# Performance work log

Measured on AMD Instinct MI355X. Metric: run time of the kernel, lower is better.

## Reference

```python
import jax, jax.numpy as jnp
import numpy as np

N = 50000        # nodes
R = 51           # enriched relations (25 fwd + 25 inverse + self-loop)
F_IN = 32        # feat_size
E = 32           # embed_size
C = 16           # num_classes
B = 30           # num_bases
NNZ = 2_000_000  # nonzeros in vertical adjacency


def _xavier(key, shape):
    # mimics nn.init.xavier_uniform_ with gain for relu (sqrt(2))
    fan_in, fan_out = shape[-2], shape[-1]
    a = np.sqrt(2.0) * np.sqrt(6.0 / (fan_in + fan_out))
    return jax.random.uniform(key, shape, jnp.float32, -a, a)


def setup_inputs() -> dict:
    key = jax.random.key(0)
    ks = jax.random.split(key, 8)
    # COO of vertical adjacency, shape (R*N, N)
    rows = jax.random.randint(ks[0], (NNZ,), 0, R * N)
    cols = jax.random.randint(ks[1], (NNZ,), 0, N)
    # row-normalized values: vals = 1 / row_degree  (sum_sparse with rows=True)
    deg = jax.ops.segment_sum(jnp.ones((NNZ,), jnp.float32), rows, num_segments=R * N)
    vals = (1.0 / jnp.maximum(deg, 1.0))[rows]
    features = jax.random.normal(ks[2], (N, F_IN), jnp.float32)
    comps1 = _xavier(ks[3], (R, B))
    bases1 = _xavier(ks[4], (B, F_IN, E))
    comps2 = _xavier(ks[5], (R, B))
    bases2 = _xavier(ks[6], (B, E, C))
    bias1 = jnp.zeros((E,), jnp.float32)
    bias2 = jnp.zeros((C,), jnp.float32)
    return {
        "features": features, "vals": vals,
        "comps1": comps1, "bases1": bases1, "bias1": bias1,
        "comps2": comps2, "bases2": bases2, "bias2": bias2,
        "rows": rows, "cols": cols,
    }


def _spmm(rows, cols, vals, x):
    # (R*N, N) sparse @ (N, f) dense -> (R*N, f)
    return jax.ops.segment_sum(vals[:, None] * x[cols], rows, num_segments=R * N)


def reference(features, vals, comps1, bases1, bias1, comps2, bases2, bias2, rows, cols):
    # layer 1: SpMM then basis-decomposed per-relation mixing
    h = _spmm(rows, cols, vals, features).reshape(R, N, F_IN)   # (r, n, f)
    w1 = jnp.einsum('rb,bfe->rfe', comps1, bases1)              # (r, f, e)
    h = jnp.einsum('rnf,rfe->ne', h, w1)                        # (n, e)
    h = jax.nn.relu(h + bias1)
    # layer 2
    h = _spmm(rows, cols, vals, h).reshape(R, N, E)             # (r, n, e)
    w2 = jnp.einsum('rb,bho->rho', comps2, bases2)              # (r, e, c)
    h = jnp.einsum('rho,rnh->no', w2, h)                        # (n, c)
    return h + bias2
```

## Files before the change

### kernel.cpp

```cpp
#include <hip/hip_runtime.h>

#define NNODES 50000
#define RREL 51
#define FIN 32
#define EDIM 32
#define CDIM 16
#define BB 30
#define NNZ_ 2000000
#define EPB 4096
#define NBUK 391
#define PCAP_MAX 2750128

typedef unsigned int uint32;
typedef unsigned short ushort;
typedef uint32 u32x2 __attribute__((ext_vector_type(2)));
typedef uint32 u32x4 __attribute__((ext_vector_type(4)));
typedef short bf16x8 __attribute__((ext_vector_type(8)));
typedef float f32x4 __attribute__((ext_vector_type(4)));
typedef float f32x16 __attribute__((ext_vector_type(16)));

static __device__ __forceinline__ uint32 pack_bf16x2(float a, float b) {
    uint32 ua = __builtin_bit_cast(uint32, a);
    uint32 ub = __builtin_bit_cast(uint32, b);
    ua += 0x7fffu + ((ua >> 16) & 1u);
    ub += 0x7fffu + ((ub >> 16) & 1u);
    return (ua >> 16) | (ub & 0xffff0000u);
}
static __device__ __forceinline__ ushort bf16_1(float x) {
    uint32 u = __builtin_bit_cast(uint32, x);
    u += 0x7fffu + ((u >> 16) & 1u);
    return (ushort)(u >> 16);
}

__global__ void k_weights2(const float* __restrict__ bases1, const float* __restrict__ bases2,
                           ushort* __restrict__ Wb1, ushort* __restrict__ Wb2) {
    int i = blockIdx.x * 256 + threadIdx.x;
    if (i < 960 * 32) {
        int e = i & 31, k = i >> 5;
        int b = k >> 5, f = k & 31;
        float v = bases1[b * 1024 + f * 32 + e];
        Wb1[((k >> 3) * 32 + e) * 8 + (k & 7)] = bf16_1(v);
    }
    if (i < 960 * 16) {
        int e = i & 15, k = i >> 4;
        int b = k >> 5, h = k & 31;
        float v = bases2[b * 512 + h * 16 + e];
        Wb2[((k >> 3) * 16 + e) * 8 + (k & 7)] = bf16_1(v);
    }
}

__global__ void k_tobf16(const float2* __restrict__ src, uint32* __restrict__ dst, int n2) {
    int i = blockIdx.x * 256 + threadIdx.x;
    if (i < n2) {
        float2 f = src[i];
        dst[i] = pack_bf16x2(f.x, f.y);
    }
}

__global__ __launch_bounds__(1024) void k_bukhist(const int* __restrict__ rows,
                                                  int* __restrict__ buk_cnt) {
    __shared__ int lc[NBUK];
    int t = threadIdx.x;
    if (t < NBUK) lc[t] = 0;
    __syncthreads();
    size_t k = (size_t)blockIdx.x * EPB + (size_t)t * 4;
    int rr[4];
    if (k + 4 <= NNZ_) {
        int4 rw = *(const int4*)(rows + k);
        rr[0] = rw.x; rr[1] = rw.y; rr[2] = rw.z; rr[3] = rw.w;
    } else {
#pragma unroll
        for (int j = 0; j < 4; j++) rr[j] = (k + j < NNZ_) ? rows[k + j] : -1;
    }
#pragma unroll
    for (int j = 0; j < 4; j++)
        if (rr[j] >= 0) {
            int rel = rr[j] / NNODES;
            int dst = rr[j] - rel * NNODES;
            atomicAdd(&lc[dst >> 7], 1);
        }
    __syncthreads();
    if (t < NBUK) atomicAdd(&buk_cnt[t], lc[t]);
}

__global__ void k_scan1(const int* __restrict__ buk_cnt, int* __restrict__ buk_base,
                        int* __restrict__ buk_cur) {
    if (threadIdx.x == 0) {
        int a = 0;
        for (int b = 0; b < NBUK; b++) { buk_base[b] = a; buk_cur[b] = a; a += buk_cnt[b]; }
        buk_base[NBUK] = a;
    }
}

__global__ __launch_bounds__(1024) void k_bucket2(const int* __restrict__ rows,
                                                  const int* __restrict__ cols,
                                                  const float* __restrict__ vals,
                                                  int* __restrict__ buk_cur,
                                                  u32x2* __restrict__ tok8,
                                                  float* __restrict__ sval_b) {
    __shared__ int bukc[NBUK], lb[NBUK], gb[NBUK];
    __shared__ int ssum[1024];
    __shared__ u32x2 st8[EPB];
    __shared__ float sv[EPB];
    int t = threadIdx.x;
    size_t base = (size_t)blockIdx.x * EPB;
    int total = (int)(((size_t)NNZ_ - base < (size_t)EPB) ? ((size_t)NNZ_ - base) : (size_t)EPB);
    if (t < NBUK) bukc[t] = 0;
    __syncthreads();
    size_t k = base + (size_t)t * 4;
    int bv[4]; uint32 tx[4], ty[4]; float vv[4];
    if (k + 4 <= NNZ_) {
        int4 rw = *(const int4*)(rows + k);
        int4 cw = *(const int4*)(cols + k);
        float4 vw = *(const float4*)(vals + k);
        int rr[4] = {rw.x, rw.y, rw.z, rw.w};
        int cc[4] = {cw.x, cw.y, cw.z, cw.w};
        vv[0] = vw.x; vv[1] = vw.y; vv[2] = vw.z; vv[3] = vw.w;
#pragma unroll
        for (int j = 0; j < 4; j++) {
            int rel = rr[j] / NNODES;
            int dst = rr[j] - rel * NNODES;
            bv[j] = dst >> 7;
            tx[j] = (uint32)dst | ((uint32)rel << 16);
            ty[j] = (uint32)cc[j] | ((uint32)rel << 16);
        }
    } else {
#pragma unroll
        for (int j = 0; j < 4; j++) {
            if (k + j < NNZ_) {
                int r = rows[k + j];
                int rel = r / NNODES;
                int dst = r - rel * NNODES;
                bv[j] = dst >> 7;
                tx[j] = (uint32)dst | ((uint32)rel << 16);
                ty[j] = (uint32)cols[k + j] | ((uint32)rel << 16);
                vv[j] = vals[k + j];
            } else bv[j] = -1;
        }
    }
#pragma unroll
    for (int j = 0; j < 4; j++)
        if (bv[j] >= 0) atomicAdd(&bukc[bv[j]], 1);
    __syncthreads();
    int v = (t < NBUK) ? bukc[t] : 0;
    ssum[t] = v;
    __syncthreads();
    for (int off = 1; off < 1024; off <<= 1) {
        int u = (t >= off) ? ssum[t - off] : 0;
        __syncthreads();
        ssum[t] += u;
        __syncthreads();
    }
    if (t < NBUK) { lb[t] = ssum[t] - v; gb[t] = atomicAdd(&buk_cur[t], v); }
    __syncthreads();
    if (t < NBUK) bukc[t] = 0;
    __syncthreads();
#pragma unroll
    for (int j = 0; j < 4; j++) {
        if (bv[j] >= 0) {
            int slot = lb[bv[j]] + atomicAdd(&bukc[bv[j]], 1);
            u32x2 w; w.x = tx[j]; w.y = ty[j];
            st8[slot] = w;
            sv[slot] = vv[j];
        }
    }
    __syncthreads();
    for (int s = t; s < total; s += 1024) {
        u32x2 w = st8[s];
        int bk = (int)((w.x & 0xFFFFu) >> 7);
        int pos = gb[bk] + (s - lb[bk]);
        tok8[pos] = w;
        sval_b[pos] = sv[s];
    }
}

__global__ __launch_bounds__(256) void k_rank3a(const u32x2* __restrict__ tok8,
                                                const int* __restrict__ buk_base,
                                                int* __restrict__ pbuk_cnt) {
    __shared__ int lcnt[128];
    __shared__ int tot;
    int b = blockIdx.x, t = threadIdx.x;
    if (t < 128) lcnt[t] = 0;
    if (t == 0) tot = 0;
    __syncthreads();
    int lo = buk_base[b], hi = buk_base[b + 1];
    for (int i = lo + t; i < hi; i += 256) atomicAdd(&lcnt[tok8[i].x & 127], 1);
    __syncthreads();
    if (t < 128) atomicAdd(&tot, (lcnt[t] + 15) & ~15);
    __syncthreads();
    if (t == 0) pbuk_cnt[b] = tot;
}

__global__ void k_scan2(const int* __restrict__ pbuk_cnt, int* __restrict__ pbuk_base) {
    if (threadIdx.x == 0) {
        int a = 0;
        for (int b = 0; b < NBUK; b++) { pbuk_base[b] = a; a += pbuk_cnt[b]; }
        pbuk_base[NBUK] = a;
    }
}

__global__ __launch_bounds__(256) void k_place(const u32x2* __restrict__ tok8,
                                               const float* __restrict__ sval_b,
                                               const int* __restrict__ buk_base,
                                               const int* __restrict__ pbuk_base,
                                               int* __restrict__ pdst_base,
                                               uint32* __restrict__ pe_sr,
                                               float* __restrict__ pe_val) {
    __shared__ int lcnt[128], lexc[128], lrank[128], ssc[128];
    int b = blockIdx.x, t = threadIdx.x;
    int lo = buk_base[b], hi = buk_base[b + 1], pb = pbuk_base[b];
    if (t < 128) { lcnt[t] = 0; lrank[t] = 0; }
    __syncthreads();
    for (int i = lo + t; i < hi; i += 256) atomicAdd(&lcnt[tok8[i].x & 127], 1);
    __syncthreads();
    int v = 0;
    if (t < 128) { v = (lcnt[t] + 15) & ~15; ssc[t] = v; }
    __syncthreads();
    for (int off = 1; off < 128; off <<= 1) {
        int u = (t >= off && t < 128) ? ssc[t - off] : 0;
        __syncthreads();
        if (t < 128) ssc[t] += u;
        __syncthreads();
    }
    if (t < 128) {
        lexc[t] = ssc[t] - v;
        int d = (b << 7) + t;
        if (d <= NNODES) pdst_base[d] = pb + lexc[t];
    }
    __syncthreads();
    for (int i = lo + t; i < hi; i += 256) {
        u32x2 w = tok8[i];
        int dl = (int)(w.x & 127u);
        int pos = pb + lexc[dl] + atomicAdd(&lrank[dl], 1);
        pe_sr[pos] = w.y;
        pe_val[pos] = sval_b[i];
    }
    if (t < 128) {
        int s0 = pb + lexc[t] + lcnt[t];
        int s1 = pb + lexc[t] + ((lcnt[t] + 15) & ~15);
        for (int i = s0; i < s1; i++) { pe_sr[i] = 0u; pe_val[i] = 0.f; }
    }
}

template <int FO, bool RELU, bool BF16OUT>
__global__ __launch_bounds__(256) void k_fused(const uint32* __restrict__ pe_sr,
                                               const float* __restrict__ pe_val,
                                               const int* __restrict__ pdst_base,
                                               const u32x4* __restrict__ Xb,
                                               const u32x4* __restrict__ Wb,
                                               const float* __restrict__ comps,
                                               const float* __restrict__ bias,
                                               void* __restrict__ outp) {
    __shared__ ushort comps_lb[RREL * 32];
    __shared__ uint32 eds[4][64];
    __shared__ float edv[4][64];
    __shared__ __align__(16) ushort xst[4][4][512];
    __shared__ __align__(16) ushort ubuf[4][4][968];
    int t = threadIdx.x, lane = t & 63, wv = t >> 6;
    for (int i = t; i < RREL * 32; i += 256) {
        int r = i >> 5, b = i & 31;
        comps_lb[i] = (b < BB) ? bf16_1(comps[r * BB + b]) : (ushort)0;
    }
    __syncthreads();
    int m = lane & 31, hf = lane >> 5, k0 = hf * 8;
    int ln15 = lane & 15, quad = lane >> 4;
    int d0 = (blockIdx.x * 4 + wv) * 8;
    if (d0 >= NNODES) return;

    auto ccprep = [&](int wi) -> u32x4 {
        float cc[8];
#pragma unroll
        for (int j = 0; j < 8; j++) {
            uint32 sr = eds[wv][wi * 16 + k0 + j];
            float vv = edv[wv][wi * 16 + k0 + j];
            uint32 cu = (uint32)comps_lb[((sr >> 16) << 5) | m] << 16;
            cc[j] = vv * __builtin_bit_cast(float, cu);
        }
        u32x4 r = { pack_bf16x2(cc[0], cc[1]), pack_bf16x2(cc[2], cc[3]),
                    pack_bf16x2(cc[4], cc[5]), pack_bf16x2(cc[6], cc[7]) };
        return r;
    };
    auto dowin = [&](int wi, u32x4 avq, f32x16 a) -> f32x16 {
        const ushort* xs = &xst[wv][wi][0];
        uint32 b0 = (uint32)xs[(k0 + 0) * 32 + m] | ((uint32)xs[(k0 + 1) * 32 + m] << 16);
        uint32 b1 = (uint32)xs[(k0 + 2) * 32 + m] | ((uint32)xs[(k0 + 3) * 32 + m] << 16);
        uint32 b2 = (uint32)xs[(k0 + 4) * 32 + m] | ((uint32)xs[(k0 + 5) * 32 + m] << 16);
        uint32 b3 = (uint32)xs[(k0 + 6) * 32 + m] | ((uint32)xs[(k0 + 7) * 32 + m] << 16);
        u32x4 bvq = { b0, b1, b2, b3 };
        return __builtin_amdgcn_mfma_f32_32x32x16_bf16(
            __builtin_bit_cast(bf16x8, avq), __builtin_bit_cast(bf16x8, bvq), a, 0, 0, 0);
    };

    int base0 = pdst_base[d0];
    uint32 pvs = __builtin_nontemporal_load(&pe_sr[base0 + lane]);
    float  pvv = __builtin_nontemporal_load(&pe_val[base0 + lane]);
    u32x4 gx0, gx1, gx2, gx3;
    {
        int s0_ = __shfl((int)pvs, (lane >> 2), 64);
        gx0 = Xb[(size_t)((uint32)s0_ & 0xFFFFu) * 4 + (lane & 3)];
        int s1_ = __shfl((int)pvs, 16 + (lane >> 2), 64);
        gx1 = Xb[(size_t)((uint32)s1_ & 0xFFFFu) * 4 + (lane & 3)];
        int s2_ = __shfl((int)pvs, 32 + (lane >> 2), 64);
        gx2 = Xb[(size_t)((uint32)s2_ & 0xFFFFu) * 4 + (lane & 3)];
        int s3_ = __shfl((int)pvs, 48 + (lane >> 2), 64);
        gx3 = Xb[(size_t)((uint32)s3_ & 0xFFFFu) * 4 + (lane & 3)];
    }

#pragma unroll 1
    for (int batch = 0; batch < 2; batch++) {
        int db = d0 + batch * 4;
#pragma unroll 1
        for (int s = 0; s < 4; s++) {
            int d = db + s;
            int lo = pdst_base[d], segEnd = pdst_base[d + 1];
            f32x16 acc;
#pragma unroll
            for (int i = 0; i < 16; i++) acc[i] = 0.f;
#pragma unroll 1
            for (int c0 = lo; c0 < segEnd; c0 += 64) {
                eds[wv][lane] = pvs;
                edv[wv][lane] = pvv;
                int nxt = c0 + 64; if (nxt > segEnd) nxt = segEnd;
                uint32 npvs = __builtin_nontemporal_load(&pe_sr[nxt + lane]);
                float  npvv = __builtin_nontemporal_load(&pe_val[nxt + lane]);
                int nwin = (segEnd - c0) >> 4;
                if (nwin > 4) nwin = 4;
                u32x4 av0, av1, av2, av3;
                av0 = ccprep(0);
                if (nwin > 1) av1 = ccprep(1);
                if (nwin > 2) av2 = ccprep(2);
                if (nwin > 3) av3 = ccprep(3);
                *(u32x4*)&xst[wv][0][lane * 8] = gx0;
                if (nwin > 1) *(u32x4*)&xst[wv][1][lane * 8] = gx1;
                if (nwin > 2) *(u32x4*)&xst[wv][2][lane * 8] = gx2;
                if (nwin > 3) *(u32x4*)&xst[wv][3][lane * 8] = gx3;
                acc = dowin(0, av0, acc);
                if (nwin > 1) acc = dowin(1, av1, acc);
                if (nwin > 2) acc = dowin(2, av2, acc);
                if (nwin > 3) acc = dowin(3, av3, acc);
                {
                    int s0_ = __shfl((int)npvs, (lane >> 2), 64);
                    gx0 = Xb[(size_t)((uint32)s0_ & 0xFFFFu) * 4 + (lane & 3)];
                    int s1_ = __shfl((int)npvs, 16 + (lane >> 2), 64);
                    gx1 = Xb[(size_t)((uint32)s1_ & 0xFFFFu) * 4 + (lane & 3)];
                    int s2_ = __shfl((int)npvs, 32 + (lane >> 2), 64);
                    gx2 = Xb[(size_t)((uint32)s2_ & 0xFFFFu) * 4 + (lane & 3)];
                    int s3_ = __shfl((int)npvs, 48 + (lane >> 2), 64);
                    gx3 = Xb[(size_t)((uint32)s3_ & 0xFFFFu) * 4 + (lane & 3)];
                }
                pvs = npvs; pvv = npvv;
            }
#pragma unroll
            for (int r = 0; r < 16; r++) {
                int b = (r & 3) + 8 * (r >> 2) + 4 * hf;
                float vme = acc[r];
                float vot = __shfl_xor(vme, 1, 64);
                if (b < BB && !(m & 1)) {
                    *(uint32*)&ubuf[wv][s][b * 32 + m] = pack_bf16x2(vme, vot);
                }
            }
        }
        const int NT = FO / 16;
        f32x4 a2[NT];
#pragma unroll
        for (int tt = 0; tt < NT; tt++)
#pragma unroll
            for (int i = 0; i < 4; i++) a2[tt][i] = 0.f;
#pragma unroll 6
        for (int ks = 0; ks < 30; ks++) {
            bf16x8 af = *(const bf16x8*)&ubuf[wv][ln15 & 3][ks * 32 + quad * 8];
#pragma unroll
            for (int tt = 0; tt < NT; tt++) {
                bf16x8 bf2 = __builtin_bit_cast(bf16x8, Wb[(ks * 4 + quad) * FO + ln15 + 16 * tt]);
                a2[tt] = __builtin_amdgcn_mfma_f32_16x16x32_bf16(af, bf2, a2[tt], 0, 0, 0);
            }
        }
        if (quad == 0) {
#pragma unroll
            for (int r = 0; r < 4; r++) {
                int dst = db + r;
                if (dst < NNODES) {
                    if (BF16OUT) {
                        ushort* hp = (ushort*)outp;
#pragma unroll
                        for (int tt = 0; tt < NT; tt++) {
                            float o = a2[tt][r] + bias[ln15 + 16 * tt];
                            if (RELU) o = fmaxf(o, 0.f);
                            hp[(size_t)dst * FO + ln15 + 16 * tt] = bf16_1(o);
                        }
                    } else {
                        float o = a2[0][r] + bias[ln15];
                        if (RELU) o = fmaxf(o, 0.f);
                        ((float*)outp)[(size_t)dst * FO + ln15] = o;
                    }
                }
            }
        }
    }
}

extern "C" void kernel_launch(void* const* d_in, const int* in_sizes, int n_in,
                              void* d_out, int out_size, void* d_ws, size_t ws_size,
                              hipStream_t stream) {
    const float* features = (const float*)d_in[0];
    const float* vals     = (const float*)d_in[1];
    const float* comps1   = (const float*)d_in[2];
    const float* bases1   = (const float*)d_in[3];
    const float* bias1    = (const float*)d_in[4];
    const float* comps2   = (const float*)d_in[5];
    const float* bases2   = (const float*)d_in[6];
    const float* bias2    = (const float*)d_in[7];
    const int*   rows     = (const int*)d_in[8];
    const int*   cols     = (const int*)d_in[9];
    float* out = (float*)d_out;

    float* ws = (float*)d_ws;
    size_t o = 0;
    ushort* Wb1 = (ushort*)(ws + o); o += 960 * 32 / 2;
    ushort* Wb2 = (ushort*)(ws + o); o += 960 * 16 / 2;
    uint32* Xb  = (uint32*)(ws + o); o += (size_t)NNODES * 16;
    uint32* h1b = (uint32*)(ws + o); o += (size_t)NNODES * 16;
    uint32* pe_sr  = (uint32*)(ws + o); o += PCAP_MAX;
    float*  pe_val = (float*)(ws + o);  o += PCAP_MAX;
    int* pdst_base = (int*)(ws + o); o += NNODES + 8;
    int* buk_cnt   = (int*)(ws + o); o += NBUK;
    int* buk_base  = (int*)(ws + o); o += NBUK + 1;
    int* buk_cur   = (int*)(ws + o); o += NBUK;
    int* pbuk_cnt  = (int*)(ws + o); o += NBUK;
    int* pbuk_base = (int*)(ws + o); o += NBUK + 1;
    o = (o + 1) & ~(size_t)1;
    u32x2* tok8 = (u32x2*)(ws + o); o += 2 * (size_t)NNZ_;
    float* sval_b = (float*)(ws + o); o += (size_t)NNZ_;

    const int NB = (NNZ_ + EPB - 1) / EPB;

    hipMemsetAsync(buk_cnt, 0, NBUK * sizeof(int), stream);

    k_weights2<<<(960 * 32 + 255) / 256, 256, 0, stream>>>(bases1, bases2, Wb1, Wb2);
    k_tobf16<<<(NNODES * FIN / 2 + 255) / 256, 256, 0, stream>>>((const float2*)features, Xb,
                                                                 NNODES * FIN / 2);
    k_bukhist<<<NB, 1024, 0, stream>>>(rows, buk_cnt);
    k_scan1<<<1, 64, 0, stream>>>(buk_cnt, buk_base, buk_cur);
    k_bucket2<<<NB, 1024, 0, stream>>>(rows, cols, vals, buk_cur, tok8, sval_b);
    k_rank3a<<<NBUK, 256, 0, stream>>>(tok8, buk_base, pbuk_cnt);
    k_scan2<<<1, 64, 0, stream>>>(pbuk_cnt, pbuk_base);
    k_place<<<NBUK, 256, 0, stream>>>(tok8, sval_b, buk_base, pbuk_base, pdst_base, pe_sr, pe_val);

    k_fused<EDIM, true, true><<<(NNODES + 31) / 32, 256, 0, stream>>>(
        pe_sr, pe_val, pdst_base, (const u32x4*)Xb, (const u32x4*)Wb1, comps1, bias1, h1b);
    k_fused<CDIM, false, false><<<(NNODES + 31) / 32, 256, 0, stream>>>(
        pe_sr, pe_val, pdst_base, (const u32x4*)h1b, (const u32x4*)Wb2, comps2, bias2, out);
}
```

Baseline: 361.2 us.

## Merge rank and place passes with atomic allocation and parallelize bucket scan

Removes the separate per-bucket padded-count kernel and its serial scan. Each place block now reserves its output range with an atomic bump allocator and records explicit per-destination start and end offsets. Empty destinations get a minimum 16-slot padded segment, so the padded buffer capacity is raised. The first bucket scan becomes a wavefront shuffle scan instead of a single-thread loop. Together these cut two kernel launches, one pass over the bucketed tokens, and serial scan latency, but destination segments are no longer in node order, which can hurt locality in the fused SpMM kernels.

```diff
diff --git a/kernel.cpp b/kernel.cpp
--- a/kernel.cpp
+++ b/kernel.cpp
@@ -9,7 +9,7 @@
 #define NNZ_ 2000000
 #define EPB 4096
 #define NBUK 391
-#define PCAP_MAX 2750128
+#define PCAP_MAX 2800128
 
 typedef unsigned int uint32;
 typedef unsigned short ushort;
@@ -85,11 +85,22 @@
 
 __global__ void k_scan1(const int* __restrict__ buk_cnt, int* __restrict__ buk_base,
                         int* __restrict__ buk_cur) {
-    if (threadIdx.x == 0) {
-        int a = 0;
-        for (int b = 0; b < NBUK; b++) { buk_base[b] = a; buk_cur[b] = a; a += buk_cnt[b]; }
-        buk_base[NBUK] = a;
-    }
+    int t = threadIdx.x;
+    int carry = 0;
+    for (int c = 0; c < NBUK; c += 64) {
+        int idx = c + t;
+        int v = (idx < NBUK) ? buk_cnt[idx] : 0;
+        int sum = v;
+#pragma unroll
+        for (int off = 1; off < 64; off <<= 1) {
+            int u = __shfl_up(sum, off, 64);
+            if (t >= off) sum += u;
+        }
+        int exc = carry + sum - v;
+        if (idx < NBUK) { buk_base[idx] = exc; buk_cur[idx] = exc; }
+        carry += __shfl(sum, 63, 64);
+    }
+    if (t == 0) buk_base[NBUK] = carry;
 }
 
 __global__ __launch_bounds__(1024) void k_bucket2(const int* __restrict__ rows,
@@ -174,47 +185,30 @@
     }
 }
 
-__global__ __launch_bounds__(256) void k_rank3a(const u32x2* __restrict__ tok8,
+__global__ __launch_bounds__(256) void k_place3(const u32x2* __restrict__ tok8,
+                                                const float* __restrict__ sval_b,
                                                 const int* __restrict__ buk_base,
-                                                int* __restrict__ pbuk_cnt) {
-    __shared__ int lcnt[128];
-    __shared__ int tot;
+                                                int* __restrict__ alloc_cur,
+                                                int* __restrict__ pdst_base,
+                                                int* __restrict__ pdst_end,
+                                                uint32* __restrict__ pe_sr,
+                                                float* __restrict__ pe_val) {
+    __shared__ int lcnt[128], lexc[128], lrank[128], ssc[128];
+    __shared__ int bbase;
     int b = blockIdx.x, t = threadIdx.x;
-    if (t < 128) lcnt[t] = 0;
-    if (t == 0) tot = 0;
-    __syncthreads();
     int lo = buk_base[b], hi = buk_base[b + 1];
+    if (t < 128) { lcnt[t] = 0; lrank[t] = 0; }
+    __syncthreads();
     for (int i = lo + t; i < hi; i += 256) atomicAdd(&lcnt[tok8[i].x & 127], 1);
     __syncthreads();
-    if (t < 128) atomicAdd(&tot, (lcnt[t] + 15) & ~15);
-    __syncthreads();
-    if (t == 0) pbuk_cnt[b] = tot;
-}
-
-__global__ void k_scan2(const int* __restrict__ pbuk_cnt, int* __restrict__ pbuk_base) {
-    if (threadIdx.x == 0) {
-        int a = 0;
-        for (int b = 0; b < NBUK; b++) { pbuk_base[b] = a; a += pbuk_cnt[b]; }
-        pbuk_base[NBUK] = a;
-    }
-}
-
-__global__ __launch_bounds__(256) void k_place(const u32x2* __restrict__ tok8,
-                                               const float* __restrict__ sval_b,
-                                               const int* __restrict__ buk_base,
-                                               const int* __restrict__ pbuk_base,
-                                               int* __restrict__ pdst_base,
-                                               uint32* __restrict__ pe_sr,
-                                               float* __restrict__ pe_val) {
-    __shared__ int lcnt[128], lexc[128], lrank[128], ssc[128];
-    int b = blockIdx.x, t = threadIdx.x;
-    int lo = buk_base[b], hi = buk_base[b + 1], pb = pbuk_base[b];
-    if (t < 128) { lcnt[t] = 0; lrank[t] = 0; }
-    __syncthreads();
-    for (int i = lo + t; i < hi; i += 256) atomicAdd(&lcnt[tok8[i].x & 127], 1);
-    __syncthreads();
     int v = 0;
-    if (t < 128) { v = (lcnt[t] + 15) & ~15; ssc[t] = v; }
+    int d = (b << 7) + t;
+    if (t < 128) {
+        v = (lcnt[t] + 15) & ~15;
+        if (d < NNODES && v == 0) v = 16;
+        if (d >= NNODES) v = 0;
+        ssc[t] = v;
+    }
     __syncthreads();
     for (int off = 1; off < 128; off <<= 1) {
         int u = (t >= off && t < 128) ? ssc[t - off] : 0;
@@ -222,22 +216,27 @@
         if (t < 128) ssc[t] += u;
         __syncthreads();
     }
+    if (t == 0) bbase = atomicAdd(alloc_cur, ssc[127]);
+    __syncthreads();
     if (t < 128) {
         lexc[t] = ssc[t] - v;
-        int d = (b << 7) + t;
-        if (d <= NNODES) pdst_base[d] = pb + lexc[t];
+        if (d < NNODES) {
+            pdst_base[d] = bbase + lexc[t];
+            pdst_end[d]  = bbase + ssc[t];
+        }
     }
     __syncthreads();
     for (int i = lo + t; i < hi; i += 256) {
         u32x2 w = tok8[i];
+        float sv = sval_b[i];
         int dl = (int)(w.x & 127u);
-        int pos = pb + lexc[dl] + atomicAdd(&lrank[dl], 1);
+        int pos = bbase + lexc[dl] + atomicAdd(&lrank[dl], 1);
         pe_sr[pos] = w.y;
-        pe_val[pos] = sval_b[i];
-    }
-    if (t < 128) {
-        int s0 = pb + lexc[t] + lcnt[t];
-        int s1 = pb + lexc[t] + ((lcnt[t] + 15) & ~15);
+        pe_val[pos] = sv;
+    }
+    if (t < 128 && d < NNODES) {
+        int s0 = bbase + lexc[t] + lcnt[t];
+        int s1 = bbase + lexc[t] + v;
         for (int i = s0; i < s1; i++) { pe_sr[i] = 0u; pe_val[i] = 0.f; }
     }
 }
@@ -246,6 +245,7 @@
 __global__ __launch_bounds__(256) void k_fused(const uint32* __restrict__ pe_sr,
                                                const float* __restrict__ pe_val,
                                                const int* __restrict__ pdst_base,
+                                               const int* __restrict__ pdst_end,
                                                const u32x4* __restrict__ Xb,
                                                const u32x4* __restrict__ Wb,
                                                const float* __restrict__ comps,
@@ -312,7 +312,7 @@
 #pragma unroll 1
         for (int s = 0; s < 4; s++) {
             int d = db + s;
-            int lo = pdst_base[d], segEnd = pdst_base[d + 1];
+            int lo = pdst_base[d], segEnd = pdst_end[d];
             f32x16 acc;
 #pragma unroll
             for (int i = 0; i < 16; i++) acc[i] = 0.f;
@@ -423,18 +423,18 @@
     uint32* pe_sr  = (uint32*)(ws + o); o += PCAP_MAX;
     float*  pe_val = (float*)(ws + o);  o += PCAP_MAX;
     int* pdst_base = (int*)(ws + o); o += NNODES + 8;
+    int* pdst_end  = (int*)(ws + o); o += NNODES + 8;
     int* buk_cnt   = (int*)(ws + o); o += NBUK;
+    int* alloc_cur = (int*)(ws + o); o += 1;
     int* buk_base  = (int*)(ws + o); o += NBUK + 1;
     int* buk_cur   = (int*)(ws + o); o += NBUK;
-    int* pbuk_cnt  = (int*)(ws + o); o += NBUK;
-    int* pbuk_base = (int*)(ws + o); o += NBUK + 1;
     o = (o + 1) & ~(size_t)1;
     u32x2* tok8 = (u32x2*)(ws + o); o += 2 * (size_t)NNZ_;
     float* sval_b = (float*)(ws + o); o += (size_t)NNZ_;
 
     const int NB = (NNZ_ + EPB - 1) / EPB;
 
-    hipMemsetAsync(buk_cnt, 0, NBUK * sizeof(int), stream);
+    hipMemsetAsync(buk_cnt, 0, (NBUK + 1) * sizeof(int), stream);
 
     k_weights2<<<(960 * 32 + 255) / 256, 256, 0, stream>>>(bases1, bases2, Wb1, Wb2);
     k_tobf16<<<(NNODES * FIN / 2 + 255) / 256, 256, 0, stream>>>((const float2*)features, Xb,
@@ -442,12 +442,11 @@
     k_bukhist<<<NB, 1024, 0, stream>>>(rows, buk_cnt);
     k_scan1<<<1, 64, 0, stream>>>(buk_cnt, buk_base, buk_cur);
     k_bucket2<<<NB, 1024, 0, stream>>>(rows, cols, vals, buk_cur, tok8, sval_b);
-    k_rank3a<<<NBUK, 256, 0, stream>>>(tok8, buk_base, pbuk_cnt);
-    k_scan2<<<1, 64, 0, stream>>>(pbuk_cnt, pbuk_base);
-    k_place<<<NBUK, 256, 0, stream>>>(tok8, sval_b, buk_base, pbuk_base, pdst_base, pe_sr, pe_val);
+    k_place3<<<NBUK, 256, 0, stream>>>(tok8, sval_b, buk_base, alloc_cur, pdst_base, pdst_end,
+                                       pe_sr, pe_val);
 
     k_fused<EDIM, true, true><<<(NNODES + 31) / 32, 256, 0, stream>>>(
-        pe_sr, pe_val, pdst_base, (const u32x4*)Xb, (const u32x4*)Wb1, comps1, bias1, h1b);
+        pe_sr, pe_val, pdst_base, pdst_end, (const u32x4*)Xb, (const u32x4*)Wb1, comps1, bias1, h1b);
     k_fused<CDIM, false, false><<<(NNODES + 31) / 32, 256, 0, stream>>>(
-        pe_sr, pe_val, pdst_base, (const u32x4*)h1b, (const u32x4*)Wb2, comps2, bias2, out);
-}
+        pe_sr, pe_val, pdst_base, pdst_end, (const u32x4*)h1b, (const u32x4*)Wb2, comps2, bias2, out);
+}
```

Result: faster. 331.2 us (-8.3%).
